# Kernel tuning notes

Hardware: AMD Instinct MI355X
Metric: run time of the kernel (lower is better)

Reference implementation:

```python
import jax, jax.numpy as jnp
import numpy as np

B, S, D, E, K = 4, 2048, 2048, 64, 2

def setup_inputs() -> dict:
    key = jax.random.key(0)
    k1, k2, k3, k4 = jax.random.split(key, 4)
    x = jax.random.normal(k1, (B, S, D), dtype=jnp.float32)
    W = jax.random.normal(k2, (E, D), dtype=jnp.float32) * 0.02  # gate_linear.weight
    noise_weight = jax.random.normal(k3, (E,), dtype=jnp.float32) * 0.02
    noise = jax.random.normal(k4, (B, S, E), dtype=jnp.float32)  # torch.randn_like(logits), noisy_std=1.0
    return {"x": x, "W": W, "noise_weight": noise_weight, "noise": noise, "k": K}

def reference(x, W, noise_weight, noise, k):
    # logits = x @ W.T  -> [B, S, E]
    logits = jnp.einsum('bsd,ed->bse', x, W)
    # noise injection: randn * noisy_std(=1.0) * noise_weight (per-expert scale)
    logits_noisy = logits + noise * noise_weight
    # top-k over experts
    top_vals, top_idx = jax.lax.top_k(logits_noisy, k)  # [B, S, k]
    # softmax over a tensor that is -inf everywhere except the top-k slots is
    # exactly: zeros everywhere, softmax(top_vals) scattered into the top-k slots.
    probs = jax.nn.softmax(top_vals, axis=-1)  # [B, S, k]
    n_tok = B * S
    rows = jnp.arange(n_tok)[:, None]  # [n_tok, 1]
    gated = jnp.zeros((n_tok, E), dtype=logits.dtype)
    gated = gated.at[rows, top_idx.reshape(n_tok, k)].set(probs.reshape(n_tok, k))
    gated = gated.reshape(B, S, E)
    return gated, top_idx, top_vals
```

## Files before the change

kernel.cpp:

```cpp
#include <hip/hip_runtime.h>
#include <math.h>

#define NTOK 8192
#define DDIM 2048
#define NEXP 64
#define MT   16
#define BK   256
#define NCH  (DDIM / BK)
#define XSTR 264
#define CSTR 66

typedef _Float16 f16x8 __attribute__((ext_vector_type(8)));
typedef float    f32x4 __attribute__((ext_vector_type(4)));

#define GATED_SZ (NTOK * NEXP)
#define IDX_OFF  GATED_SZ
#define VALS_OFF (GATED_SZ + NTOK * 2)

#define NKSTEP (DDIM / 32)
#define NTILE  (NEXP / 16)
#define BFRAG_HALVES ((size_t)NKSTEP * NTILE * 64 * 8)

__global__ void pack_b_kernel(const float* __restrict__ W,
                              _Float16* __restrict__ Bh,
                              _Float16* __restrict__ Bl)
{
    const int tid  = blockIdx.x * blockDim.x + threadIdx.x;
    const int lane = tid & 63;
    const int fid  = tid >> 6;
    const int ks   = fid >> 2;
    const int nt   = fid & 3;
    const int e    = nt * 16 + (lane & 15);
    const int k    = ks * 32 + (lane >> 4) * 8;
    const float* src = W + (size_t)e * DDIM + k;

    f16x8 hi, lo;
#pragma unroll
    for (int j = 0; j < 8; ++j) {
        const float v = src[j];
        const _Float16 h = (_Float16)v;
        hi[j] = h;
        lo[j] = (_Float16)((v - (float)h) * 4096.f);
    }
    *(f16x8*)(Bh + (size_t)tid * 8) = hi;
    *(f16x8*)(Bl + (size_t)tid * 8) = lo;
}

#define BFRAG(base, ks) (*(const f16x8*)((base) + ((((size_t)(ks)) * 4 + nt) * 64 + lane) * 8))

__global__ __launch_bounds__(512, 4) void gate_kernel(
    const float* __restrict__ x,
    const _Float16* __restrict__ Bh,
    const _Float16* __restrict__ Bl,
    const float* __restrict__ noise_w,
    const float* __restrict__ noise,
    float* __restrict__ out)
{
    __shared__ _Float16 xh[2][MT * XSTR];
    __shared__ _Float16 xl[2][MT * XSTR];
    __shared__ float    cbuf[2][MT * CSTR];

    const int tid  = threadIdx.x;
    const int lane = tid & 63;
    const int w    = __builtin_amdgcn_readfirstlane(tid >> 6);
    const int h    = w >> 2;
    const int nt   = w & 3;
    const int tokBase = blockIdx.x * MT;

    const int srow = tid >> 5;
    const int scol = tid & 31;
    const float* xsrc = x + (size_t)(tokBase + srow) * DDIM + scol * 8;

    const int q = lane >> 4;
    const int m = lane & 15;
    const int abase = m * XSTR + h * (BK / 2) + q * 8;

    f32x4 acc_hh = {0.f, 0.f, 0.f, 0.f};
    f32x4 acc_lo = {0.f, 0.f, 0.f, 0.f};

    float4 st0 = *(const float4*)(xsrc);
    float4 st1 = *(const float4*)(xsrc + 4);

    for (int c = 0; c < NCH; ++c) {
        const int p = c & 1;

        {
            f16x8 h8, l8;
            const float vv[8] = {st0.x, st0.y, st0.z, st0.w,
                                 st1.x, st1.y, st1.z, st1.w};
#pragma unroll
            for (int j = 0; j < 8; ++j) {
                const _Float16 hh = (_Float16)vv[j];
                h8[j] = hh;
                l8[j] = (_Float16)((vv[j] - (float)hh) * 4096.f);
            }
            *(f16x8*)&xh[p][srow * XSTR + scol * 8] = h8;
            *(f16x8*)&xl[p][srow * XSTR + scol * 8] = l8;
        }

        if (c + 1 < NCH) {
            st0 = *(const float4*)(xsrc + (size_t)(c + 1) * BK);
            st1 = *(const float4*)(xsrc + (size_t)(c + 1) * BK + 4);
        }

        __syncthreads();

        const int ksb = c * 8 + h * 4;
#pragma unroll
        for (int stp = 0; stp < 4; ++stp) {
            const f16x8 bh = BFRAG(Bh, ksb + stp);
            const f16x8 bl = BFRAG(Bl, ksb + stp);
            const f16x8 ah = *(const f16x8*)&xh[p][abase + stp * 32];
            const f16x8 al = *(const f16x8*)&xl[p][abase + stp * 32];
            acc_hh = __builtin_amdgcn_mfma_f32_16x16x32_f16(ah, bh, acc_hh, 0, 0, 0);
            acc_lo = __builtin_amdgcn_mfma_f32_16x16x32_f16(ah, bl, acc_lo, 0, 0, 0);
            acc_lo = __builtin_amdgcn_mfma_f32_16x16x32_f16(al, bh, acc_lo, 0, 0, 0);
        }
    }

    {
        const int e = nt * 16 + m;
#pragma unroll
        for (int r = 0; r < 4; ++r) {
            const int t = q * 4 + r;
            cbuf[h][t * CSTR + e] = acc_hh[r] + acc_lo[r] * (1.f / 4096.f);
        }
    }
    __syncthreads();

    const float nwv = noise_w[lane];
#pragma unroll
    for (int i = 0; i < 2; ++i) {
        const int t   = w * 2 + i;
        const int tok = tokBase + t;
        const int e   = lane;

        float v = cbuf[0][t * CSTR + e] + cbuf[1][t * CSTR + e]
                + noise[(size_t)tok * NEXP + e] * nwv;

        float m1 = v; int i1 = e;
#pragma unroll
        for (int sh = 32; sh > 0; sh >>= 1) {
            float ov = __shfl_xor(m1, sh, 64);
            int   oi = __shfl_xor(i1, sh, 64);
            if (ov > m1 || (ov == m1 && oi < i1)) { m1 = ov; i1 = oi; }
        }
        float vm = (e == i1) ? -INFINITY : v;
        float m2 = vm; int i2 = e;
#pragma unroll
        for (int sh = 32; sh > 0; sh >>= 1) {
            float ov = __shfl_xor(m2, sh, 64);
            int   oi = __shfl_xor(i2, sh, 64);
            if (ov > m2 || (ov == m2 && oi < i2)) { m2 = ov; i2 = oi; }
        }

        const float e2  = expf(m2 - m1);
        const float inv = 1.f / (1.f + e2);
        const float p1  = inv;
        const float p2  = e2 * inv;

        float gval = 0.f;
        if (e == i1) gval = p1;
        else if (e == i2) gval = p2;
        out[(size_t)tok * NEXP + e] = gval;

        if (lane == 0) {
            out[IDX_OFF  + tok * 2 + 0] = (float)i1;
            out[IDX_OFF  + tok * 2 + 1] = (float)i2;
            out[VALS_OFF + tok * 2 + 0] = m1;
            out[VALS_OFF + tok * 2 + 1] = m2;
        }
    }
}

extern "C" void kernel_launch(void* const* d_in, const int* in_sizes, int n_in,
                              void* d_out, int out_size, void* d_ws, size_t ws_size,
                              hipStream_t stream) {
    const float* x      = (const float*)d_in[0];
    const float* W      = (const float*)d_in[1];
    const float* nw     = (const float*)d_in[2];
    const float* noise  = (const float*)d_in[3];
    float* out = (float*)d_out;

    _Float16* Bh = (_Float16*)d_ws;
    _Float16* Bl = Bh + BFRAG_HALVES;

    hipLaunchKernelGGL(pack_b_kernel, dim3(64), dim3(256), 0, stream, W, Bh, Bl);

    hipLaunchKernelGGL(gate_kernel, dim3(NTOK / MT), dim3(512), 0, stream,
                       x, Bh, Bl, nw, noise, out);
}
```

Baseline: 113.8 us.

## Split K across all eight waves, drop LDS staging and W prepack kernel

Each of the eight waves now owns a 256-wide K slice and computes all four expert tiles. It loads x and W directly from global memory into registers and converts them to hi/lo fp16 in place, so the LDS double buffering, per-chunk barriers and the separate W packing kernel launch are gone. Partial sums from the eight waves are reduced through a larger LDS buffer before top-k. The cost is that every block re-reads and re-converts W from fp32 on each K step, which adds global/L2 traffic and conversion ALU work. It also uses strided, less coalesced loads for x.

```diff
diff --git a/kernel.cpp b/kernel.cpp
--- a/kernel.cpp
+++ b/kernel.cpp
@@ -5,125 +5,83 @@
 #define DDIM 2048
 #define NEXP 64
 #define MT   16
-#define BK   256
-#define NCH  (DDIM / BK)
-#define XSTR 264
-#define CSTR 66
-
-typedef _Float16 f16x8 __attribute__((ext_vector_type(8)));
-typedef float    f32x4 __attribute__((ext_vector_type(4)));
+#define PSTR 68
 
 #define GATED_SZ (NTOK * NEXP)
 #define IDX_OFF  GATED_SZ
 #define VALS_OFF (GATED_SZ + NTOK * 2)
 
-#define NKSTEP (DDIM / 32)
-#define NTILE  (NEXP / 16)
-#define BFRAG_HALVES ((size_t)NKSTEP * NTILE * 64 * 8)
+typedef _Float16 f16x8 __attribute__((ext_vector_type(8)));
+typedef float    f32x4 __attribute__((ext_vector_type(4)));
 
-__global__ void pack_b_kernel(const float* __restrict__ W,
-                              _Float16* __restrict__ Bh,
-                              _Float16* __restrict__ Bl)
+static __device__ __forceinline__ void cvt_hilo(float4 v0, float4 v1,
+                                                f16x8& h8, f16x8& l8)
 {
-    const int tid  = blockIdx.x * blockDim.x + threadIdx.x;
-    const int lane = tid & 63;
-    const int fid  = tid >> 6;
-    const int ks   = fid >> 2;
-    const int nt   = fid & 3;
-    const int e    = nt * 16 + (lane & 15);
-    const int k    = ks * 32 + (lane >> 4) * 8;
-    const float* src = W + (size_t)e * DDIM + k;
-
-    f16x8 hi, lo;
+    const float vv[8] = {v0.x, v0.y, v0.z, v0.w, v1.x, v1.y, v1.z, v1.w};
 #pragma unroll
     for (int j = 0; j < 8; ++j) {
-        const float v = src[j];
-        const _Float16 h = (_Float16)v;
-        hi[j] = h;
-        lo[j] = (_Float16)((v - (float)h) * 4096.f);
+        const _Float16 hh = (_Float16)vv[j];
+        h8[j] = hh;
+        l8[j] = (_Float16)((vv[j] - (float)hh) * 4096.f);
     }
-    *(f16x8*)(Bh + (size_t)tid * 8) = hi;
-    *(f16x8*)(Bl + (size_t)tid * 8) = lo;
 }
-
-#define BFRAG(base, ks) (*(const f16x8*)((base) + ((((size_t)(ks)) * 4 + nt) * 64 + lane) * 8))
 
 __global__ __launch_bounds__(512, 4) void gate_kernel(
     const float* __restrict__ x,
-    const _Float16* __restrict__ Bh,
-    const _Float16* __restrict__ Bl,
+    const float* __restrict__ W,
     const float* __restrict__ noise_w,
     const float* __restrict__ noise,
     float* __restrict__ out)
 {
-    __shared__ _Float16 xh[2][MT * XSTR];
-    __shared__ _Float16 xl[2][MT * XSTR];
-    __shared__ float    cbuf[2][MT * CSTR];
+    __shared__ float cbuf[8][MT * PSTR];
 
     const int tid  = threadIdx.x;
     const int lane = tid & 63;
     const int w    = __builtin_amdgcn_readfirstlane(tid >> 6);
-    const int h    = w >> 2;
-    const int nt   = w & 3;
     const int tokBase = blockIdx.x * MT;
-
-    const int srow = tid >> 5;
-    const int scol = tid & 31;
-    const float* xsrc = x + (size_t)(tokBase + srow) * DDIM + scol * 8;
 
     const int q = lane >> 4;
     const int m = lane & 15;
-    const int abase = m * XSTR + h * (BK / 2) + q * 8;
 
-    f32x4 acc_hh = {0.f, 0.f, 0.f, 0.f};
-    f32x4 acc_lo = {0.f, 0.f, 0.f, 0.f};
+    const float* asrc = x + (size_t)(tokBase + m) * DDIM + (size_t)w * 256 + q * 8;
+    const float* bsrc = W + (size_t)m * DDIM + (size_t)w * 256 + q * 8;
 
-    float4 st0 = *(const float4*)(xsrc);
-    float4 st1 = *(const float4*)(xsrc + 4);
+    f32x4 acc_hh[4], acc_lo[4];
+#pragma unroll
+    for (int nt = 0; nt < 4; ++nt) {
+        acc_hh[nt] = (f32x4){0.f, 0.f, 0.f, 0.f};
+        acc_lo[nt] = (f32x4){0.f, 0.f, 0.f, 0.f};
+    }
 
-    for (int c = 0; c < NCH; ++c) {
-        const int p = c & 1;
+#pragma unroll 2
+    for (int s = 0; s < 8; ++s) {
+        const size_t ko = (size_t)s * 32;
 
-        {
-            f16x8 h8, l8;
-            const float vv[8] = {st0.x, st0.y, st0.z, st0.w,
-                                 st1.x, st1.y, st1.z, st1.w};
+        const float4 a0 = *(const float4*)(asrc + ko);
+        const float4 a1 = *(const float4*)(asrc + ko + 4);
+        f16x8 ah, al;
+        cvt_hilo(a0, a1, ah, al);
+
 #pragma unroll
-            for (int j = 0; j < 8; ++j) {
-                const _Float16 hh = (_Float16)vv[j];
-                h8[j] = hh;
-                l8[j] = (_Float16)((vv[j] - (float)hh) * 4096.f);
-            }
-            *(f16x8*)&xh[p][srow * XSTR + scol * 8] = h8;
-            *(f16x8*)&xl[p][srow * XSTR + scol * 8] = l8;
-        }
+        for (int nt = 0; nt < 4; ++nt) {
+            const float4 b0 = *(const float4*)(bsrc + (size_t)nt * 16 * DDIM + ko);
+            const float4 b1 = *(const float4*)(bsrc + (size_t)nt * 16 * DDIM + ko + 4);
+            f16x8 bh, bl;
+            cvt_hilo(b0, b1, bh, bl);
 
-        if (c + 1 < NCH) {
-            st0 = *(const float4*)(xsrc + (size_t)(c + 1) * BK);
-            st1 = *(const float4*)(xsrc + (size_t)(c + 1) * BK + 4);
-        }
-
-        __syncthreads();
-
-        const int ksb = c * 8 + h * 4;
-#pragma unroll
-        for (int stp = 0; stp < 4; ++stp) {
-            const f16x8 bh = BFRAG(Bh, ksb + stp);
-            const f16x8 bl = BFRAG(Bl, ksb + stp);
-            const f16x8 ah = *(const f16x8*)&xh[p][abase + stp * 32];
-            const f16x8 al = *(const f16x8*)&xl[p][abase + stp * 32];
-            acc_hh = __builtin_amdgcn_mfma_f32_16x16x32_f16(ah, bh, acc_hh, 0, 0, 0);
-            acc_lo = __builtin_amdgcn_mfma_f32_16x16x32_f16(ah, bl, acc_lo, 0, 0, 0);
-            acc_lo = __builtin_amdgcn_mfma_f32_16x16x32_f16(al, bh, acc_lo, 0, 0, 0);
+            acc_hh[nt] = __builtin_amdgcn_mfma_f32_16x16x32_f16(ah, bh, acc_hh[nt], 0, 0, 0);
+            acc_lo[nt] = __builtin_amdgcn_mfma_f32_16x16x32_f16(ah, bl, acc_lo[nt], 0, 0, 0);
+            acc_lo[nt] = __builtin_amdgcn_mfma_f32_16x16x32_f16(al, bh, acc_lo[nt], 0, 0, 0);
         }
     }
 
-    {
+#pragma unroll
+    for (int nt = 0; nt < 4; ++nt) {
         const int e = nt * 16 + m;
 #pragma unroll
         for (int r = 0; r < 4; ++r) {
             const int t = q * 4 + r;
-            cbuf[h][t * CSTR + e] = acc_hh[r] + acc_lo[r] * (1.f / 4096.f);
+            cbuf[w][t * PSTR + e] = acc_hh[nt][r] + acc_lo[nt][r] * (1.f / 4096.f);
         }
     }
     __syncthreads();
@@ -135,8 +93,11 @@
         const int tok = tokBase + t;
         const int e   = lane;
 
-        float v = cbuf[0][t * CSTR + e] + cbuf[1][t * CSTR + e]
-                + noise[(size_t)tok * NEXP + e] * nwv;
+        float v = 0.f;
+#pragma unroll
+        for (int p = 0; p < 8; ++p)
+            v += cbuf[p][t * PSTR + e];
+        v += noise[(size_t)tok * NEXP + e] * nwv;
 
         float m1 = v; int i1 = e;
 #pragma unroll
@@ -176,17 +137,13 @@
 extern "C" void kernel_launch(void* const* d_in, const int* in_sizes, int n_in,
                               void* d_out, int out_size, void* d_ws, size_t ws_size,
                               hipStream_t stream) {
-    const float* x      = (const float*)d_in[0];
-    const float* W      = (const float*)d_in[1];
-    const float* nw     = (const float*)d_in[2];
-    const float* noise  = (const float*)d_in[3];
+    const float* x     = (const float*)d_in[0];
+    const float* W     = (const float*)d_in[1];
+    const float* nw    = (const float*)d_in[2];
+    const float* noise = (const float*)d_in[3];
     float* out = (float*)d_out;
-
-    _Float16* Bh = (_Float16*)d_ws;
-    _Float16* Bl = Bh + BFRAG_HALVES;
-
-    hipLaunchKernelGGL(pack_b_kernel, dim3(64), dim3(256), 0, stream, W, Bh, Bl);
+    (void)d_ws; (void)ws_size;
 
     hipLaunchKernelGGL(gate_kernel, dim3(NTOK / MT), dim3(512), 0, stream,
-                       x, Bh, Bl, nw, noise, out);
+                       x, W, nw, noise, out);
 }
```

New measurement: 131.3 us. 1.15x slower.
